# Performance work log

Measured on AMD Instinct MI355X. Metric: run time of the kernel, lower is better.

## Reference

```python
import jax, jax.numpy as jnp
import numpy as np

B, G, K, A = 2, 50000, 32, 64  # batch, grid points, neighbors, ao_vals


def setup_inputs() -> dict:
    key = jax.random.key(0)
    k1, k2, k3, k4 = jax.random.split(key, 4)
    out = jax.random.normal(k1, (B, G, A), dtype=jnp.float32)
    # neighbor indices in [0, G]; index G points at the zero padding row
    coords_neighbors_idx = jax.random.randint(k2, (G, K), 0, G + 1, dtype=jnp.int32)
    scale = 1.0 / np.sqrt(A)
    W2 = jax.random.normal(k3, (A, A), dtype=jnp.float32) * scale
    b2 = jnp.zeros((A,), dtype=jnp.float32)
    W3 = jax.random.normal(k4, (A, A), dtype=jnp.float32) * scale
    b3 = jnp.zeros((A,), dtype=jnp.float32)
    return {"out": out, "coords_neighbors_idx": coords_neighbors_idx,
            "W2": W2, "b2": b2, "W3": W3, "b3": b3}


def reference(out, coords_neighbors_idx, W2, b2, W3, b3):
    n_batch, n_grid, n_ao = out.shape
    # pad grid axis with a zero row so index n_grid gathers zeros
    pad = jnp.concatenate([out, jnp.zeros((n_batch, 1, n_ao), out.dtype)], axis=1)
    # gather neighbors: [B, G, K, A], then sum-aggregate over neighbors
    messages = jnp.take(pad, coords_neighbors_idx, axis=1).sum(axis=2)  # [B, G, A]
    messages = messages @ W2 + b2  # dense_2 (activation=None)
    y = out + messages             # residual
    y = y @ W3 + b3                # dense_3 (activation=None)
    return y
```

## Files before the change

kernel.cpp:

```cpp
#include <hip/hip_runtime.h>
#include <hip/hip_fp16.h>


constexpr int A  = 64;
constexpr int K  = 32;
constexpr int GPB = 32;
constexpr int XS = 136;

typedef _Float16 f16x8 __attribute__((ext_vector_type(8)));
typedef float    f32x4 __attribute__((ext_vector_type(4)));

__global__ void prep_kernel(const float* __restrict__ W2, const float* __restrict__ b2,
                            const float* __restrict__ W3, const float* __restrict__ b3,
                            __half* __restrict__ WTg, float* __restrict__ bb,
                            const float2* __restrict__ out2,
                            __half2* __restrict__ packed, const int G) {
  if (blockIdx.x < 16) {
    const int e = blockIdx.x * 256 + threadIdx.x;
    const int n = e >> 6, k = e & 63;
    float acc = 0.f;
#pragma unroll
    for (int q = 0; q < A; ++q) acc = fmaf(W2[k * A + q], W3[q * A + n], acc);
    WTg[n * 128 + k]     = __float2half(acc);
    WTg[n * 128 + A + k] = __float2half(W3[k * A + n]);
    if (blockIdx.x == 0 && threadIdx.x < A) {
      const int t = threadIdx.x;
      float b = b3[t];
#pragma unroll
      for (int q = 0; q < A; ++q) b = fmaf(b2[q], W3[q * A + t], b);
      bb[t] = b;
    }
    return;
  }
  const int d = (blockIdx.x - 16) * 256 + threadIdx.x;
  const int total = (G + 1) * 64;
  if (d >= total) return;
  const int g = d >> 6, c = d & 63;
  float2 v = make_float2(0.f, 0.f);
  if (g < G) {
    const int b = c >> 5;
    v = out2[(size_t)b * (G * 32) + (size_t)g * 32 + (c & 31)];
  }
  packed[d] = __floats2half2_rn(v.x, v.y);
}

__global__ __launch_bounds__(256, 8) void fused_kernel(
    const __half2* __restrict__ packed, const int* __restrict__ nbr,
    const __half* __restrict__ WTg, const float* __restrict__ bb,
    float* __restrict__ y, const int G) {
  __shared__ __half X[64 * XS];

  const int tid = threadIdx.x;
  const int lane = tid & 63;
  const int w = __builtin_amdgcn_readfirstlane(tid >> 6);
  const int gbase = blockIdx.x * GPB;
  const int gcount = min(GPB, G - gbase);
  const int e = lane & 31;
  const int rb = (lane >> 5) * 32;

  const __half2 z = __floats2half2_rn(0.f, 0.f);

#pragma unroll
  for (int gg = 0; gg < 8; ++gg) {
    const int gl = w * 8 + gg;
    if (gl < gcount) {
      const int g = gbase + gl;
      const int* np = nbr + g * K;
      __half2 m0 = z, m1 = z, m2 = z, m3 = z;
#pragma unroll
      for (int k = 0; k < K; k += 4) {
        const __half2 u0 = packed[(size_t)np[k]     * 64 + lane];
        const __half2 u1 = packed[(size_t)np[k + 1] * 64 + lane];
        const __half2 u2 = packed[(size_t)np[k + 2] * 64 + lane];
        const __half2 u3 = packed[(size_t)np[k + 3] * 64 + lane];
        m0 = __hadd2(m0, u0);
        m1 = __hadd2(m1, u1);
        m2 = __hadd2(m2, u2);
        m3 = __hadd2(m3, u3);
      }
      const __half2 m = __hadd2(__hadd2(m0, m1), __hadd2(m2, m3));
      const __half2 o = packed[(size_t)g * 64 + lane];
      const int r = rb + gl;
      *(__half2*)&X[r * XS + 2 * e]     = m;
      *(__half2*)&X[r * XS + A + 2 * e] = o;
    }
  }
  __syncthreads();

  const int quad = lane >> 4;
  const int mn = lane & 15;
  f32x4 acc0 = {0.f, 0.f, 0.f, 0.f};
  f32x4 acc1 = {0.f, 0.f, 0.f, 0.f};
  f32x4 acc2 = {0.f, 0.f, 0.f, 0.f};
  f32x4 acc3 = {0.f, 0.f, 0.f, 0.f};
#pragma unroll
  for (int kt = 0; kt < 4; ++kt) {
    const int ko = kt * 32 + quad * 8;
    const f16x8 a = *(const f16x8*)&X[(w * 16 + mn) * XS + ko];
    const f16x8 b0 = *(const f16x8*)&WTg[(0 * 16 + mn) * 128 + ko];
    acc0 = __builtin_amdgcn_mfma_f32_16x16x32_f16(a, b0, acc0, 0, 0, 0);
    const f16x8 b1 = *(const f16x8*)&WTg[(1 * 16 + mn) * 128 + ko];
    acc1 = __builtin_amdgcn_mfma_f32_16x16x32_f16(a, b1, acc1, 0, 0, 0);
    const f16x8 b2 = *(const f16x8*)&WTg[(2 * 16 + mn) * 128 + ko];
    acc2 = __builtin_amdgcn_mfma_f32_16x16x32_f16(a, b2, acc2, 0, 0, 0);
    const f16x8 b3 = *(const f16x8*)&WTg[(3 * 16 + mn) * 128 + ko];
    acc3 = __builtin_amdgcn_mfma_f32_16x16x32_f16(a, b3, acc3, 0, 0, 0);
  }

  f32x4 accs[4] = {acc0, acc1, acc2, acc3};
#pragma unroll
  for (int nt = 0; nt < 4; ++nt) {
    const int col = nt * 16 + mn;
    const float bv = bb[col];
#pragma unroll
    for (int rg = 0; rg < 4; ++rg) {
      const int row = w * 16 + quad * 4 + rg;
      const int b = row >> 5, gl = row & 31;
      if (gl < gcount)
        y[((size_t)b * G + (gbase + gl)) * 64 + col] = accs[nt][rg] + bv;
    }
  }
}

extern "C" void kernel_launch(void* const* d_in, const int* in_sizes, int n_in,
                              void* d_out, int out_size, void* d_ws, size_t ws_size,
                              hipStream_t stream) {
  const float* out = (const float*)d_in[0];
  const int*   nbr = (const int*)d_in[1];
  const float* W2  = (const float*)d_in[2];
  const float* b2  = (const float*)d_in[3];
  const float* W3  = (const float*)d_in[4];
  const float* b3  = (const float*)d_in[5];
  float* y = (float*)d_out;
  const int G = in_sizes[1] / K;

  __half2* packed = (__half2*)d_ws;
  const size_t packedBytes = (size_t)(G + 1) * 64 * sizeof(__half2);
  __half* WTg = (__half*)((char*)d_ws + packedBytes);
  float* bb = (float*)((char*)d_ws + packedBytes + 8192 * sizeof(__half));

  const int packTotal = (G + 1) * 64;
  const int prepBlocks = 16 + (packTotal + 255) / 256;
  prep_kernel<<<prepBlocks, 256, 0, stream>>>(W2, b2, W3, b3, WTg, bb,
                                              (const float2*)out, packed, G);

  const int blocks = (G + GPB - 1) / GPB;
  fused_kernel<<<blocks, 256, 0, stream>>>(packed, nbr, WTg, bb, y, G);
}
```

Before: 141.3 us.

## Segment neighbor gather by index range to improve cache locality

Each wave now loads all 32 neighbor indices into lanes up front. It then walks the packed table in 8 index-range segments, using a ballot and readlane to gather only the neighbors that fall in the current segment. The aim is that blocks running concurrently touch the same slice of the table at the same time, which should raise L2 hit rates on the random gathers. In exchange it adds ballot and loop overhead, serial scalar readlanes, and divergent variable-length loops. It also changes the fp16 summation order.

```diff
diff --git a/kernel.cpp b/kernel.cpp
--- a/kernel.cpp
+++ b/kernel.cpp
@@ -2,10 +2,11 @@
 #include <hip/hip_fp16.h>
 
 
-constexpr int A  = 64;
-constexpr int K  = 32;
+constexpr int A   = 64;
+constexpr int K   = 32;
 constexpr int GPB = 32;
-constexpr int XS = 136;
+constexpr int XS  = 136;
+constexpr int NSEG = 8;
 
 typedef _Float16 f16x8 __attribute__((ext_vector_type(8)));
 typedef float    f32x4 __attribute__((ext_vector_type(4)));
@@ -57,32 +58,70 @@
   const int gcount = min(GPB, G - gbase);
   const int e = lane & 31;
   const int rb = (lane >> 5) * 32;
+  const int kl = lane & 31;
 
   const __half2 z = __floats2half2_rn(0.f, 0.f);
+
+  int vidx[8];
+#pragma unroll
+  for (int gg = 0; gg < 8; ++gg) {
+    const int gl = w * 8 + gg;
+    const int g = gbase + (gl < gcount ? gl : 0);
+    vidx[gg] = nbr[(size_t)g * K + kl];
+  }
+
+  __half2 msum[8];
+#pragma unroll
+  for (int gg = 0; gg < 8; ++gg) msum[gg] = z;
+
+  const int seglen = (G + NSEG) / NSEG;
+
+  for (int seg = 0; seg < NSEG; ++seg) {
+    const int lo = seg * seglen;
+#pragma unroll
+    for (int gg = 0; gg < 8; ++gg) {
+      const int gl = w * 8 + gg;
+      const int g = gbase + (gl < gcount ? gl : 0);
+      if (gl < gcount && g >= lo && g < lo + seglen) {
+        const int r = rb + gl;
+        *(__half2*)&X[r * XS + A + 2 * e] = packed[(size_t)g * 64 + lane];
+      }
+      const bool inseg = ((unsigned)(vidx[gg] - lo)) < (unsigned)seglen;
+      unsigned int mask = (unsigned int)__ballot(inseg);
+      __half2 a0 = z, a1 = z, a2 = z, a3 = z;
+      while (__popc(mask) >= 4) {
+        const int k0 = __builtin_ctz(mask); mask &= mask - 1;
+        const int k1 = __builtin_ctz(mask); mask &= mask - 1;
+        const int k2 = __builtin_ctz(mask); mask &= mask - 1;
+        const int k3 = __builtin_ctz(mask); mask &= mask - 1;
+        const int i0 = __builtin_amdgcn_readlane(vidx[gg], k0);
+        const int i1 = __builtin_amdgcn_readlane(vidx[gg], k1);
+        const int i2 = __builtin_amdgcn_readlane(vidx[gg], k2);
+        const int i3 = __builtin_amdgcn_readlane(vidx[gg], k3);
+        const __half2 u0 = packed[(size_t)i0 * 64 + lane];
+        const __half2 u1 = packed[(size_t)i1 * 64 + lane];
+        const __half2 u2 = packed[(size_t)i2 * 64 + lane];
+        const __half2 u3 = packed[(size_t)i3 * 64 + lane];
+        a0 = __hadd2(a0, u0);
+        a1 = __hadd2(a1, u1);
+        a2 = __hadd2(a2, u2);
+        a3 = __hadd2(a3, u3);
+      }
+      while (mask) {
+        const int k0 = __builtin_ctz(mask); mask &= mask - 1;
+        const int i0 = __builtin_amdgcn_readlane(vidx[gg], k0);
+        a0 = __hadd2(a0, packed[(size_t)i0 * 64 + lane]);
+      }
+      msum[gg] = __hadd2(msum[gg], __hadd2(__hadd2(a0, a1), __hadd2(a2, a3)));
+    }
+  }
 
 #pragma unroll
   for (int gg = 0; gg < 8; ++gg) {
     const int gl = w * 8 + gg;
     if (gl < gcount) {
-      const int g = gbase + gl;
-      const int* np = nbr + g * K;
-      __half2 m0 = z, m1 = z, m2 = z, m3 = z;
-#pragma unroll
-      for (int k = 0; k < K; k += 4) {
-        const __half2 u0 = packed[(size_t)np[k]     * 64 + lane];
-        const __half2 u1 = packed[(size_t)np[k + 1] * 64 + lane];
-        const __half2 u2 = packed[(size_t)np[k + 2] * 64 + lane];
-        const __half2 u3 = packed[(size_t)np[k + 3] * 64 + lane];
-        m0 = __hadd2(m0, u0);
-        m1 = __hadd2(m1, u1);
-        m2 = __hadd2(m2, u2);
-        m3 = __hadd2(m3, u3);
-      }
-      const __half2 m = __hadd2(__hadd2(m0, m1), __hadd2(m2, m3));
-      const __half2 o = packed[(size_t)g * 64 + lane];
       const int r = rb + gl;
-      *(__half2*)&X[r * XS + 2 * e]     = m;
-      *(__half2*)&X[r * XS + A + 2 * e] = o;
+      *(__half2*)&X[r * XS + 2 * e] = msum[gg];
     }
   }
   __syncthreads();
```

Result: slower. 167.3 us (+18.4%).
